# Kernel optimization log

Hardware: AMD Instinct MI355X
Metric: run time of the kernel (lower is better)

Reference implementation:

```python
import jax, jax.numpy as jnp
import numpy as np

B, M, L, D = 4, 4, 512, 1024
N_HEAD = 16
D_HEAD = D // N_HEAD
LN_EPS = 1e-6


def setup_inputs() -> dict:
    key = jax.random.key(0)
    ks = jax.random.split(key, 9)
    s = 1.0 / np.sqrt(D)
    return {
        "q": jax.random.normal(ks[0], (B, M, L, D), dtype=jnp.float32),
        "k": jax.random.normal(ks[1], (B, M, L, D), dtype=jnp.float32),
        "qi": jax.random.normal(ks[2], (B, M, L, D), dtype=jnp.float32),
        "mask": jax.random.randint(ks[3], (B, M, L, L), 0, 2, dtype=jnp.int32),
        "w_qs": jax.random.normal(ks[4], (D, D), dtype=jnp.float32) * s,
        "w_qis": jax.random.normal(ks[5], (D, D), dtype=jnp.float32) * s,
        "w_fc": jax.random.normal(ks[6], (D, D), dtype=jnp.float32) * s,
        "ln_g": jnp.ones((D,), dtype=jnp.float32),
        "ln_b": jnp.zeros((D,), dtype=jnp.float32),
    }


def _l2_normalize(x):
    # normaliseE: divide by sqrt(sum of squares) over the last axis (no eps)
    return x / jnp.sqrt(jnp.sum(x * x, axis=-1, keepdims=True))


def _softmax2d(attn):
    # softmax jointly over the (doc, key) axes = axes (1, 4) of [B,M,H,Lq,Lk]
    m = jnp.max(attn, axis=(1, 4), keepdims=True)
    e = jnp.exp(attn - m)
    return e / jnp.sum(e, axis=(1, 4), keepdims=True)


def reference(q, k, qi, mask, w_qs, w_qis, w_fc, ln_g, ln_b):
    del k  # unused by the original forward
    b, m, lq, d = q.shape
    residual = q

    # LayerNorm(d_model, eps=1e-6) on q only
    mu = jnp.mean(q, axis=-1, keepdims=True)
    var = jnp.mean(jnp.square(q - mu), axis=-1, keepdims=True)
    qn = (q - mu) / jnp.sqrt(var + LN_EPS) * ln_g + ln_b

    # projections (bias-free) and head split -> [B,M,H,L,d_head]
    qh = (qn @ w_qs).reshape(b, m, lq, N_HEAD, D_HEAD)
    qih = (qi @ w_qis).reshape(b, m, qi.shape[2], N_HEAD, D_HEAD)
    qh = jnp.swapaxes(_l2_normalize(qh), 2, 3)
    qih = jnp.swapaxes(_l2_normalize(qih), 2, 3)

    # cosine-similarity scores (BSM=True -> no temperature scaling)
    attn = jnp.einsum("bmhqd,bmhkd->bmhqk", qh, qih)

    # mask broadcast over heads (the torch transpose dance is equivalent)
    attn = jnp.where(mask[:, :, None, :, :] == 0, -1e9, attn)

    attn = _softmax2d(attn)  # dropout is identity at eval

    out = jnp.einsum("bmhqk,bmhkd->bmhqd", attn, qih)
    out = jnp.swapaxes(out, 2, 3).reshape(b, m, lq, d)
    out = out @ w_fc + residual
    return out, attn
```

## Files before the change

kernel.cpp:

```cpp
#include <hip/hip_runtime.h>
#include <hip/hip_bf16.h>
#include <cstdint>
#include <cstddef>

#define Bq 4
#define Mq 4
#define Lseq 512
#define Dmod 1024
#define Hq 16
#define DHq 64

using bf16 = __bf16;
using bf16x4 = __attribute__((ext_vector_type(4))) __bf16;
using bf16x8 = __attribute__((ext_vector_type(8))) __bf16;
using f32x4 = __attribute__((ext_vector_type(4))) float;
using u64 = unsigned long long;

__device__ __forceinline__ void gld_lds16(const bf16* g, bf16* l) {
  __builtin_amdgcn_global_load_lds(
      (const __attribute__((address_space(1))) void*)g,
      (__attribute__((address_space(3))) void*)l, 16, 0, 0);
}

template <int WAVES_M, int WAVES_N, int WTM, int WTN>
__device__ __forceinline__ void gemm_core(const bf16* __restrict__ A,
                                          const bf16* __restrict__ Bt,
                                          int K, int lda, int ldb,
                                          bf16* As, bf16* Bs,
                                          f32x4 (&acc)[WTM][WTN]) {
  constexpr int BM = WAVES_M * WTM * 16;
  constexpr int BN = WAVES_N * WTN * 16;
  constexpr int IA = BM / 64;
  constexpr int IB = BN / 64;

  const int t = threadIdx.x;
  const int lane = t & 63;
  const int wave = t >> 6;
  const int wm = wave % WAVES_M;
  const int wn = wave / WAVES_M;
  const int r = t >> 2;
  const int c8 = (t & 3) * 8;
  const int fr = lane & 15;
  const int fk = (lane >> 4) * 8;

  const bf16* Ab = A + (size_t)r * lda + c8;
  const bf16* Bb = Bt + (size_t)r * ldb + c8;

  for (int k0 = 0; k0 < K; k0 += 32) {
    if (k0) __syncthreads();
#pragma unroll
    for (int i = 0; i < IA; ++i)
      gld_lds16(Ab + (size_t)i * 64 * lda + k0, As + i * 2048 + t * 8);
#pragma unroll
    for (int i = 0; i < IB; ++i)
      gld_lds16(Bb + (size_t)i * 64 * ldb + k0, Bs + i * 2048 + t * 8);
    asm volatile("s_waitcnt vmcnt(0)" ::: "memory");
    __syncthreads();

    bf16x8 af[WTM], bfv[WTN];
#pragma unroll
    for (int i = 0; i < WTM; ++i)
      af[i] = *(const bf16x8*)(As + (wm * WTM * 16 + i * 16 + fr) * 32 + fk);
#pragma unroll
    for (int j = 0; j < WTN; ++j)
      bfv[j] = *(const bf16x8*)(Bs + (wn * WTN * 16 + j * 16 + fr) * 32 + fk);
#pragma unroll
    for (int i = 0; i < WTM; ++i)
#pragma unroll
      for (int j = 0; j < WTN; ++j)
        acc[i][j] = __builtin_amdgcn_mfma_f32_16x16x32_bf16(af[i], bfv[j],
                                                            acc[i][j], 0, 0, 0);
  }
}

__global__ __launch_bounds__(256) void gemm_bt_128_l2n(
    const bf16* __restrict__ A, const bf16* __restrict__ Bt,
    bf16* __restrict__ C, int K, int lda, int ldb, int ldc) {
  __shared__ __align__(16) bf16 As[128 * 32];
  __shared__ __align__(16) bf16 Bs[128 * 32];
  f32x4 acc[4][4] = {};
  const bf16* Ab = A + (size_t)blockIdx.y * 128 * lda;
  const bf16* Bb = Bt + (size_t)blockIdx.x * 128 * ldb;
  gemm_core<2, 2, 4, 4>(Ab, Bb, K, lda, ldb, As, Bs, acc);

  const int t = threadIdx.x, lane = t & 63, wave = t >> 6;
  const int wm = wave & 1, wn = wave >> 1;
  const int cr = (lane >> 4) * 4, cc = lane & 15;
  const size_t row0 = (size_t)blockIdx.y * 128 + wm * 64;
  const size_t col0 = (size_t)blockIdx.x * 128 + wn * 64;
#pragma unroll
  for (int i = 0; i < 4; ++i)
#pragma unroll
    for (int rg = 0; rg < 4; ++rg) {
      float ss = 0.0f;
#pragma unroll
      for (int j = 0; j < 4; ++j) ss += acc[i][j][rg] * acc[i][j][rg];
      ss += __shfl_xor(ss, 1);
      ss += __shfl_xor(ss, 2);
      ss += __shfl_xor(ss, 4);
      ss += __shfl_xor(ss, 8);
      const float r = (ss > 0.0f) ? rsqrtf(ss) : 0.0f;
#pragma unroll
      for (int j = 0; j < 4; ++j)
        C[(row0 + i * 16 + cr + rg) * ldc + col0 + j * 16 + cc] =
            (bf16)(acc[i][j][rg] * r);
    }
}

__global__ __launch_bounds__(256) void gemm_bt_resid(
    const bf16* __restrict__ A, const bf16* __restrict__ Bt,
    const float* __restrict__ resid, float* __restrict__ C, int K, int lda,
    int ldb, int ldc) {
  __shared__ __align__(16) bf16 As[128 * 32];
  __shared__ __align__(16) bf16 Bs[128 * 32];
  f32x4 acc[4][4] = {};
  const bf16* Ab = A + (size_t)blockIdx.y * 128 * lda;
  const bf16* Bb = Bt + (size_t)blockIdx.x * 128 * ldb;
  gemm_core<2, 2, 4, 4>(Ab, Bb, K, lda, ldb, As, Bs, acc);

  const int t = threadIdx.x, lane = t & 63, wave = t >> 6;
  const int wm = wave & 1, wn = wave >> 1;
  const int cr = (lane >> 4) * 4, cc = lane & 15;
  const size_t row0 = (size_t)blockIdx.y * 128 + wm * 64;
  const size_t col0 = (size_t)blockIdx.x * 128 + wn * 64;
#pragma unroll
  for (int i = 0; i < 4; ++i)
#pragma unroll
    for (int j = 0; j < 4; ++j)
#pragma unroll
      for (int rg = 0; rg < 4; ++rg) {
        size_t idx = (row0 + i * 16 + cr + rg) * ldc + col0 + j * 16 + cc;
        float rv = __builtin_nontemporal_load(resid + idx);
        __builtin_nontemporal_store(acc[i][j][rg] + rv, C + idx);
      }
}

__global__ __launch_bounds__(256) void mask_to_bits(
    const int* __restrict__ mask, u64* __restrict__ mb) {
  const int wid = blockIdx.x * 4 + (threadIdx.x >> 6);
  const int lane = threadIdx.x & 63;
#pragma unroll
  for (int it = 0; it < 16; ++it) {
    const size_t W = (size_t)wid * 16 + it;
    const u64 b = __ballot(mask[W * 64 + lane] != 0);
    if (lane == 0) mb[W] = b;
  }
}

__device__ __forceinline__ void attn_swizzle(int flat, int& z, int& q0) {
  const int slot = flat >> 3;
  z = (flat & 7) * 32 + (slot >> 2);
  q0 = (slot & 3) * 128;
}

__global__ __launch_bounds__(256) void denom_kernel(
    const bf16* __restrict__ qh, const bf16* __restrict__ qih,
    const u64* __restrict__ mb, float* __restrict__ denom) {
  __shared__ __align__(16) bf16 Qs[128 * 64];
  __shared__ __align__(16) bf16 Ks[2][64 * 64];

  int z, q0;
  attn_swizzle(blockIdx.x, z, q0);
  const int bm = z >> 4, h = z & 15;

  const int t = threadIdx.x;
  const int lane = t & 63;
  const int wave = t >> 6;
  const int wm = wave & 1, wn = wave >> 1;
  const int fr = lane & 15;
  const int hi = lane >> 4;
  const int sr = t >> 3;
  const int sc = t & 7;

  const bf16* qh_b = qh + ((size_t)bm * Lseq + q0) * Dmod + h * DHq;
  const bf16* qih_b = qih + (size_t)bm * Lseq * Dmod + h * DHq;
  const u64* mrow = mb + (size_t)bm * Lseq * 8;

#pragma unroll
  for (int s = 0; s < 4; ++s) {
    const int r = s * 32 + sr;
    gld_lds16(qh_b + (size_t)r * Dmod + ((sc ^ (r & 7)) << 3),
              Qs + s * 2048 + t * 8);
  }
#pragma unroll
  for (int s = 0; s < 2; ++s) {
    const int r = s * 32 + sr;
    gld_lds16(qih_b + (size_t)r * Dmod + ((sc ^ (r & 7)) << 3),
              Ks[0] + s * 2048 + t * 8);
  }

  float racc[4][4] = {};

  for (int kt = 0; kt < 8; ++kt) {
    asm volatile("s_waitcnt vmcnt(0)" ::: "memory");
    __syncthreads();

    if (kt < 7) {
      const int kv1 = (kt + 1) * 64;
#pragma unroll
      for (int s = 0; s < 2; ++s) {
        const int r = s * 32 + sr;
        gld_lds16(qih_b + (size_t)(kv1 + r) * Dmod + ((sc ^ (r & 7)) << 3),
                  Ks[(kt + 1) & 1] + s * 2048 + t * 8);
      }
    }

    u64 mw[4][4];
#pragma unroll
    for (int i = 0; i < 4; ++i)
#pragma unroll
      for (int rg = 0; rg < 4; ++rg)
        mw[i][rg] =
            mrow[(size_t)(q0 + wm * 64 + i * 16 + hi * 4 + rg) * 8 + kt];

    const bf16* Kc = Ks[kt & 1];
    f32x4 acc_s[4][2] = {};
    __builtin_amdgcn_s_setprio(1);
#pragma unroll
    for (int kk = 0; kk < 2; ++kk) {
      bf16x8 bq[4], bk[2];
#pragma unroll
      for (int i = 0; i < 4; ++i) {
        const int row = wm * 64 + i * 16 + fr;
        bq[i] = *(const bf16x8*)(Qs + row * 64 +
                                 ((((kk << 2) + hi) ^ (row & 7)) << 3));
      }
#pragma unroll
      for (int j = 0; j < 2; ++j) {
        const int row = wn * 32 + j * 16 + fr;
        bk[j] = *(const bf16x8*)(Kc + row * 64 +
                                 ((((kk << 2) + hi) ^ (row & 7)) << 3));
      }
#pragma unroll
      for (int i = 0; i < 4; ++i)
#pragma unroll
        for (int j = 0; j < 2; ++j)
          acc_s[i][j] = __builtin_amdgcn_mfma_f32_16x16x32_bf16(
              bq[i], bk[j], acc_s[i][j], 0, 0, 0);
    }
    __builtin_amdgcn_s_setprio(0);

#pragma unroll
    for (int i = 0; i < 4; ++i)
#pragma unroll
      for (int rg = 0; rg < 4; ++rg) {
        const unsigned hw = (unsigned)(mw[i][rg] >> (wn * 32));
#pragma unroll
        for (int j = 0; j < 2; ++j)
          if ((hw >> (j * 16 + fr)) & 1)
            racc[i][rg] += __expf(acc_s[i][j][rg] - 1.0f);
      }
  }

  float* dp = denom + ((size_t)(bm >> 2) * Hq + h) * Lseq + q0 + wm * 64;
#pragma unroll
  for (int i = 0; i < 4; ++i)
#pragma unroll
    for (int rg = 0; rg < 4; ++rg) {
      float rs = racc[i][rg];
      rs += __shfl_xor(rs, 1);
      rs += __shfl_xor(rs, 2);
      rs += __shfl_xor(rs, 4);
      rs += __shfl_xor(rs, 8);
      if (fr == 0) atomicAdd(dp + i * 16 + hi * 4 + rg, rs);
    }
}

__global__ __launch_bounds__(256) void fused_attn(
    const bf16* __restrict__ qh, const bf16* __restrict__ qih,
    const bf16* __restrict__ qih_t, const u64* __restrict__ mb,
    const float* __restrict__ denom, float* __restrict__ attn,
    bf16* __restrict__ outh) {
  __shared__ __align__(16) bf16 Qs[128 * 64];
  __shared__ __align__(16) bf16 Ks[2][64 * 64];
  __shared__ __align__(16) bf16 Vs[2][64 * 64];
  __shared__ __align__(16) bf16 Ps[2][128 * 64];

  int z, q0;
  attn_swizzle(blockIdx.x, z, q0);
  const int bm = z >> 4, h = z & 15;

  const int t = threadIdx.x;
  const int lane = t & 63;
  const int wave = t >> 6;
  const int wm = wave & 1, wn = wave >> 1;
  const int fr = lane & 15;
  const int hi = lane >> 4;
  const int sr = t >> 3;
  const int sc = t & 7;

  const bf16* qh_b = qh + ((size_t)bm * Lseq + q0) * Dmod + h * DHq;
  const bf16* qih_b = qih + (size_t)bm * Lseq * Dmod + h * DHq;
  const bf16* vt_b = qih_t + (size_t)z * DHq * Lseq;
  const u64* mrow = mb + (size_t)bm * Lseq * 8;
  float* arow = attn + (size_t)z * Lseq * Lseq;

#pragma unroll
  for (int s = 0; s < 4; ++s) {
    const int r = s * 32 + sr;
    gld_lds16(qh_b + (size_t)r * Dmod + ((sc ^ (r & 7)) << 3),
              Qs + s * 2048 + t * 8);
  }
#pragma unroll
  for (int s = 0; s < 2; ++s) {
    const int r = s * 32 + sr;
    gld_lds16(qih_b + (size_t)r * Dmod + ((sc ^ (r & 7)) << 3),
              Ks[0] + s * 2048 + t * 8);
    gld_lds16(vt_b + (size_t)r * Lseq + ((sc ^ (r & 7)) << 3),
              Vs[0] + s * 2048 + t * 8);
  }

  const float* drow = denom + ((size_t)(bm >> 2) * Hq + h) * Lseq + q0;
  float invd[4][4];
#pragma unroll
  for (int i = 0; i < 4; ++i)
#pragma unroll
    for (int rg = 0; rg < 4; ++rg) {
      const float d = drow[wm * 64 + i * 16 + hi * 4 + rg];
      invd[i][rg] = (d > 0.0f) ? 1.0f / d : 0.0f;
    }

  f32x4 acc_o[4][2] = {};

  for (int kt = 0; kt < 8; ++kt) {
    const int kv0 = kt * 64;
    asm volatile("s_waitcnt vmcnt(0)" ::: "memory");
    __syncthreads();

    if (kt < 7) {
      const int kv1 = kv0 + 64;
#pragma unroll
      for (int s = 0; s < 2; ++s) {
        const int r = s * 32 + sr;
        gld_lds16(qih_b + (size_t)(kv1 + r) * Dmod + ((sc ^ (r & 7)) << 3),
                  Ks[(kt + 1) & 1] + s * 2048 + t * 8);
        gld_lds16(vt_b + (size_t)r * Lseq + kv1 + ((sc ^ (r & 7)) << 3),
                  Vs[(kt + 1) & 1] + s * 2048 + t * 8);
      }
    }

    u64 mw[4][4];
#pragma unroll
    for (int i = 0; i < 4; ++i)
#pragma unroll
      for (int rg = 0; rg < 4; ++rg)
        mw[i][rg] =
            mrow[(size_t)(q0 + wm * 64 + i * 16 + hi * 4 + rg) * 8 + kt];

    const bf16* Kc = Ks[kt & 1];
    f32x4 acc_s[4][2] = {};
    __builtin_amdgcn_s_setprio(1);
#pragma unroll
    for (int kk = 0; kk < 2; ++kk) {
      bf16x8 bq[4], bk[2];
#pragma unroll
      for (int i = 0; i < 4; ++i) {
        const int row = wm * 64 + i * 16 + fr;
        bq[i] = *(const bf16x8*)(Qs + row * 64 +
                                 ((((kk << 2) + hi) ^ (row & 7)) << 3));
      }
#pragma unroll
      for (int j = 0; j < 2; ++j) {
        const int row = wn * 32 + j * 16 + fr;
        bk[j] = *(const bf16x8*)(Kc + row * 64 +
                                 ((((kk << 2) + hi) ^ (row & 7)) << 3));
      }
#pragma unroll
      for (int i = 0; i < 4; ++i)
#pragma unroll
        for (int j = 0; j < 2; ++j)
          acc_s[i][j] = __builtin_amdgcn_mfma_f32_16x16x32_bf16(
              bq[i], bk[j], acc_s[i][j], 0, 0, 0);
    }
    __builtin_amdgcn_s_setprio(0);

    bf16* Pc = Ps[kt & 1];
#pragma unroll
    for (int i = 0; i < 4; ++i)
#pragma unroll
      for (int j = 0; j < 2; ++j)
#pragma unroll
        for (int rg = 0; rg < 4; ++rg) {
          const int ql = wm * 64 + i * 16 + hi * 4 + rg;
          const int cl = wn * 32 + j * 16 + fr;
          const unsigned hw = (unsigned)(mw[i][rg] >> (wn * 32));
          float p = 0.0f;
          if ((hw >> (j * 16 + fr)) & 1)
            p = __expf(acc_s[i][j][rg] - 1.0f) * invd[i][rg];
          __builtin_nontemporal_store(
              p, arow + (size_t)(q0 + ql) * Lseq + kv0 + cl);
          Pc[ql * 64 + (((cl >> 3) ^ (ql & 7)) << 3) + (cl & 7)] = (bf16)p;
        }
    asm volatile("s_waitcnt lgkmcnt(0)" ::: "memory");
    __builtin_amdgcn_s_barrier();

    const bf16* Vc = Vs[kt & 1];
    __builtin_amdgcn_s_setprio(1);
#pragma unroll
    for (int kk = 0; kk < 2; ++kk) {
      bf16x8 ap[4], bv[2];
#pragma unroll
      for (int i = 0; i < 4; ++i) {
        const int row = wm * 64 + i * 16 + fr;
        ap[i] = *(const bf16x8*)(Pc + row * 64 +
                                 ((((kk << 2) + hi) ^ (row & 7)) << 3));
      }
#pragma unroll
      for (int j = 0; j < 2; ++j) {
        const int row = wn * 32 + j * 16 + fr;
        bv[j] = *(const bf16x8*)(Vc + row * 64 +
                                 ((((kk << 2) + hi) ^ (row & 7)) << 3));
      }
#pragma unroll
      for (int i = 0; i < 4; ++i)
#pragma unroll
        for (int j = 0; j < 2; ++j)
          acc_o[i][j] = __builtin_amdgcn_mfma_f32_16x16x32_bf16(
              ap[i], bv[j], acc_o[i][j], 0, 0, 0);
    }
    __builtin_amdgcn_s_setprio(0);
  }

  bf16* Cb = outh + ((size_t)bm * Lseq + q0) * Dmod + h * DHq;
#pragma unroll
  for (int i = 0; i < 4; ++i)
#pragma unroll
    for (int j = 0; j < 2; ++j)
#pragma unroll
      for (int rg = 0; rg < 4; ++rg)
        Cb[(size_t)(wm * 64 + i * 16 + hi * 4 + rg) * Dmod + wn * 32 +
           j * 16 + fr] = (bf16)acc_o[i][j][rg];
}

__global__ __launch_bounds__(256) void ln_kernel(const float* __restrict__ q,
                                                 const float* __restrict__ g,
                                                 const float* __restrict__ b,
                                                 bf16* __restrict__ qn) {
  const size_t row = blockIdx.x;
  const float* x = q + row * Dmod;
  bf16* y = qn + row * Dmod;
  const int t = threadIdx.x;
  float4 v = *(const float4*)(x + t * 4);
  float s = v.x + v.y + v.z + v.w;
  float ss = v.x * v.x + v.y * v.y + v.z * v.z + v.w * v.w;
  for (int off = 32; off; off >>= 1) {
    s += __shfl_xor(s, off);
    ss += __shfl_xor(ss, off);
  }
  __shared__ float sm[8];
  const int wave = t >> 6, lane = t & 63;
  if (lane == 0) { sm[wave * 2] = s; sm[wave * 2 + 1] = ss; }
  __syncthreads();
  s = sm[0] + sm[2] + sm[4] + sm[6];
  ss = sm[1] + sm[3] + sm[5] + sm[7];
  const float mean = s * (1.0f / Dmod);
  const float var = ss * (1.0f / Dmod) - mean * mean;
  const float rstd = rsqrtf(var + 1e-6f);
  float4 gg = *(const float4*)(g + t * 4);
  float4 bb = *(const float4*)(b + t * 4);
  bf16x4 o;
  o[0] = (bf16)((v.x - mean) * rstd * gg.x + bb.x);
  o[1] = (bf16)((v.y - mean) * rstd * gg.y + bb.y);
  o[2] = (bf16)((v.z - mean) * rstd * gg.z + bb.z);
  o[3] = (bf16)((v.w - mean) * rstd * gg.w + bb.w);
  *(bf16x4*)(y + t * 4) = o;
}

__global__ __launch_bounds__(256) void cvt_f32_bf16(const float* __restrict__ in,
                                                    bf16* __restrict__ out) {
  const size_t i = ((size_t)blockIdx.x * 256 + threadIdx.x) * 4;
  float4 v = *(const float4*)(in + i);
  bf16x4 o;
  o[0] = (bf16)v.x; o[1] = (bf16)v.y; o[2] = (bf16)v.z; o[3] = (bf16)v.w;
  *(bf16x4*)(out + i) = o;
}

__global__ __launch_bounds__(256) void transpose64_f32(
    const float* __restrict__ in, bf16* __restrict__ out, int ld_in,
    int ld_out) {
  __shared__ bf16 tile[64 * 65];
  const int r0 = blockIdx.y * 64, c0 = blockIdx.x * 64;
  const int t = threadIdx.x, cl = t & 63, rq = t >> 6;
#pragma unroll
  for (int it = 0; it < 16; ++it) {
    const int rl = it * 4 + rq;
    tile[cl * 65 + rl] = (bf16)in[(size_t)(r0 + rl) * ld_in + c0 + cl];
  }
  __syncthreads();
#pragma unroll
  for (int it = 0; it < 16; ++it) {
    const int ol = it * 4 + rq;
    out[(size_t)(c0 + ol) * ld_out + r0 + cl] = tile[ol * 65 + cl];
  }
}

__global__ __launch_bounds__(256) void transpose_qih(
    const bf16* __restrict__ qih, bf16* __restrict__ qih_t) {
  __shared__ bf16 tile[64 * 65];
  const int z = blockIdx.z;
  const int bm = z >> 4, h = z & 15;
  const bf16* in = qih + (size_t)bm * Lseq * Dmod + h * DHq;
  bf16* out = qih_t + (size_t)z * DHq * Lseq;
  const int r0 = blockIdx.x * 64;
  const int t = threadIdx.x, cl = t & 63, rq = t >> 6;
#pragma unroll
  for (int it = 0; it < 16; ++it) {
    const int rl = it * 4 + rq;
    tile[cl * 65 + rl] = in[(size_t)(r0 + rl) * Dmod + cl];
  }
  __syncthreads();
#pragma unroll
  for (int it = 0; it < 16; ++it) {
    const int dh = it * 4 + rq;
    out[(size_t)dh * Lseq + r0 + cl] = tile[dh * 65 + cl];
  }
}

extern "C" void kernel_launch(void* const* d_in, const int* in_sizes, int n_in,
                              void* d_out, int out_size, void* d_ws,
                              size_t ws_size, hipStream_t stream) {
  const float* q = (const float*)d_in[0];
  const float* qi = (const float*)d_in[2];
  const int* mask = (const int*)d_in[3];
  const float* w_qs = (const float*)d_in[4];
  const float* w_qis = (const float*)d_in[5];
  const float* w_fc = (const float*)d_in[6];
  const float* ln_g = (const float*)d_in[7];
  const float* ln_b = (const float*)d_in[8];

  float* out = (float*)d_out;
  const size_t NE = (size_t)Bq * Mq * Lseq * Dmod;
  float* attn = out + NE;

  char* attnc = (char*)attn;
  bf16* qib = (bf16*)attnc;
  bf16* wqs_t = (bf16*)(attnc + (16u << 20));
  bf16* wqis_t = (bf16*)(attnc + (18u << 20));

  char* ws = (char*)d_ws;
  const size_t SZ = NE * sizeof(bf16);
  bf16* qn = (bf16*)(ws);
  bf16* qh = (bf16*)(ws + SZ);
  bf16* qih = (bf16*)(ws + 2 * SZ);
  bf16* qih_t = (bf16*)(ws + 3 * SZ);
  bf16* wfc_t = (bf16*)(ws + 4 * SZ);
  float* denom = (float*)(ws + 4 * SZ + (2u << 20));
  u64* mbits = (u64*)(ws + 4 * SZ + (4u << 20));
  bf16* outh = qn;

  const int ROWS = Bq * Mq * Lseq;

  mask_to_bits<<<1024, 256, 0, stream>>>(mask, mbits);
  cvt_f32_bf16<<<NE / 1024, 256, 0, stream>>>(qi, qib);
  transpose64_f32<<<dim3(16, 16), 256, 0, stream>>>(w_qs, wqs_t, Dmod, Dmod);
  transpose64_f32<<<dim3(16, 16), 256, 0, stream>>>(w_qis, wqis_t, Dmod, Dmod);
  transpose64_f32<<<dim3(16, 16), 256, 0, stream>>>(w_fc, wfc_t, Dmod, Dmod);
  hipMemsetAsync(denom, 0, (size_t)Bq * Hq * Lseq * sizeof(float), stream);

  ln_kernel<<<ROWS, 256, 0, stream>>>(q, ln_g, ln_b, qn);

  gemm_bt_128_l2n<<<dim3(Dmod / 128, ROWS / 128), 256, 0, stream>>>(
      qn, wqs_t, qh, Dmod, Dmod, Dmod, Dmod);
  gemm_bt_128_l2n<<<dim3(Dmod / 128, ROWS / 128), 256, 0, stream>>>(
      qib, wqis_t, qih, Dmod, Dmod, Dmod, Dmod);

  transpose_qih<<<dim3(Lseq / 64, 1, Bq * Mq * Hq), 256, 0, stream>>>(qih,
                                                                      qih_t);

  denom_kernel<<<1024, 256, 0, stream>>>(qh, qih, mbits, denom);

  fused_attn<<<1024, 256, 0, stream>>>(qh, qih, qih_t, mbits, denom, attn,
                                       outh);

  gemm_bt_resid<<<dim3(Dmod / 128, ROWS / 128), 256, 0, stream>>>(
      outh, wfc_t, q, out, Dmod, Dmod, Dmod, Dmod);
}
```

Before: 600.5 us.

## Double-buffer LDS tiles in GEMM core to overlap global loads with MFMA

The shared GEMM core now prefetches the next K-slice of the A and B tiles into a second LDS buffer while MFMAs run on the current buffer. This leaves one barrier per K step instead of two and hides global-to-LDS load latency behind compute. It also raises wave priority around the MFMA block with s_setprio. The cost is double the LDS footprint for the two GEMM kernels, which may reduce occupancy.

```diff
diff --git a/kernel.cpp b/kernel.cpp
--- a/kernel.cpp
+++ b/kernel.cpp
@@ -32,6 +32,8 @@
   constexpr int BN = WAVES_N * WTN * 16;
   constexpr int IA = BM / 64;
   constexpr int IB = BN / 64;
+  constexpr int ASZ = BM * 32;
+  constexpr int BSZ = BN * 32;
 
   const int t = threadIdx.x;
   const int lane = t & 63;
@@ -46,38 +48,56 @@
   const bf16* Ab = A + (size_t)r * lda + c8;
   const bf16* Bb = Bt + (size_t)r * ldb + c8;
 
+#pragma unroll
+  for (int i = 0; i < IA; ++i)
+    gld_lds16(Ab + (size_t)i * 64 * lda, As + i * 2048 + t * 8);
+#pragma unroll
+  for (int i = 0; i < IB; ++i)
+    gld_lds16(Bb + (size_t)i * 64 * ldb, Bs + i * 2048 + t * 8);
+
+  int cur = 0;
   for (int k0 = 0; k0 < K; k0 += 32) {
-    if (k0) __syncthreads();
-#pragma unroll
-    for (int i = 0; i < IA; ++i)
-      gld_lds16(Ab + (size_t)i * 64 * lda + k0, As + i * 2048 + t * 8);
-#pragma unroll
-    for (int i = 0; i < IB; ++i)
-      gld_lds16(Bb + (size_t)i * 64 * ldb + k0, Bs + i * 2048 + t * 8);
     asm volatile("s_waitcnt vmcnt(0)" ::: "memory");
     __syncthreads();
 
+    if (k0 + 32 < K) {
+      const int nxt = cur ^ 1;
+#pragma unroll
+      for (int i = 0; i < IA; ++i)
+        gld_lds16(Ab + (size_t)i * 64 * lda + k0 + 32,
+                  As + nxt * ASZ + i * 2048 + t * 8);
+#pragma unroll
+      for (int i = 0; i < IB; ++i)
+        gld_lds16(Bb + (size_t)i * 64 * ldb + k0 + 32,
+                  Bs + nxt * BSZ + i * 2048 + t * 8);
+    }
+
+    const bf16* Ac = As + cur * ASZ;
+    const bf16* Bc = Bs + cur * BSZ;
     bf16x8 af[WTM], bfv[WTN];
 #pragma unroll
     for (int i = 0; i < WTM; ++i)
-      af[i] = *(const bf16x8*)(As + (wm * WTM * 16 + i * 16 + fr) * 32 + fk);
+      af[i] = *(const bf16x8*)(Ac + (wm * WTM * 16 + i * 16 + fr) * 32 + fk);
 #pragma unroll
     for (int j = 0; j < WTN; ++j)
-      bfv[j] = *(const bf16x8*)(Bs + (wn * WTN * 16 + j * 16 + fr) * 32 + fk);
+      bfv[j] = *(const bf16x8*)(Bc + (wn * WTN * 16 + j * 16 + fr) * 32 + fk);
+    __builtin_amdgcn_s_setprio(1);
 #pragma unroll
     for (int i = 0; i < WTM; ++i)
 #pragma unroll
       for (int j = 0; j < WTN; ++j)
         acc[i][j] = __builtin_amdgcn_mfma_f32_16x16x32_bf16(af[i], bfv[j],
                                                             acc[i][j], 0, 0, 0);
+    __builtin_amdgcn_s_setprio(0);
+    cur ^= 1;
   }
 }
 
 __global__ __launch_bounds__(256) void gemm_bt_128_l2n(
     const bf16* __restrict__ A, const bf16* __restrict__ Bt,
     bf16* __restrict__ C, int K, int lda, int ldb, int ldc) {
-  __shared__ __align__(16) bf16 As[128 * 32];
-  __shared__ __align__(16) bf16 Bs[128 * 32];
+  __shared__ __align__(16) bf16 As[2 * 128 * 32];
+  __shared__ __align__(16) bf16 Bs[2 * 128 * 32];
   f32x4 acc[4][4] = {};
   const bf16* Ab = A + (size_t)blockIdx.y * 128 * lda;
   const bf16* Bb = Bt + (size_t)blockIdx.x * 128 * ldb;
@@ -111,8 +131,8 @@
     const bf16* __restrict__ A, const bf16* __restrict__ Bt,
     const float* __restrict__ resid, float* __restrict__ C, int K, int lda,
     int ldb, int ldc) {
-  __shared__ __align__(16) bf16 As[128 * 32];
-  __shared__ __align__(16) bf16 Bs[128 * 32];
+  __shared__ __align__(16) bf16 As[2 * 128 * 32];
+  __shared__ __align__(16) bf16 Bs[2 * 128 * 32];
   f32x4 acc[4][4] = {};
   const bf16* Ab = A + (size_t)blockIdx.y * 128 * lda;
   const bf16* Bb = Bt + (size_t)blockIdx.x * 128 * ldb;
```

Measured after the change: 581.9 us. 3.1% less time.
